# Kernel tuning notes

Hardware: AMD Instinct MI355X
Metric: run time of the kernel (lower is better)

The kernel has to match this reference:

```python
import jax, jax.numpy as jnp
import numpy as np

E = 8        # n_experts
K = 2        # top_k
D = 1024     # n_embed
H = 2048     # moe_n_hidden
B, T = 4, 2048


def setup_inputs() -> dict:
    key = jax.random.key(0)
    ks = jax.random.split(key, 6)
    s = 0.02
    return {
        "x": jax.random.normal(ks[0], (B, T, D), dtype=jnp.float32),
        "Wr": jax.random.normal(ks[1], (D, E), dtype=jnp.float32) * s,   # router weight
        "W1": jax.random.normal(ks[2], (E, D, 2 * H), dtype=jnp.float32) * s,
        "b1": jnp.zeros((E, 2 * H), dtype=jnp.float32),
        "W2": jax.random.normal(ks[3], (E, H, D), dtype=jnp.float32) * s,
        "b2": jnp.zeros((E, D), dtype=jnp.float32),
    }


def reference(x, Wr, W1, b1, W2, b2):
    b, t, d = x.shape
    # router logits (noise=0, temp=1.0)
    z = jnp.einsum('btd,de->bte', x, Wr)                 # [B,T,E]
    vals, idx = jax.lax.top_k(z, K)                      # [B,T,K]
    gates = jax.nn.softmax(vals, axis=-1)                # [B,T,K]
    # combine weights per (token, expert): sum_k gate_k * 1[idx_k == e]
    onehot = jax.nn.one_hot(idx, E, dtype=x.dtype)       # [B,T,K,E]
    comb = jnp.einsum('btk,btke->bte', gates, onehot).reshape(b * t, E)
    xf = x.reshape(b * t, d)                             # [N,D]
    out = jnp.zeros_like(xf)
    for e in range(E):  # fixed small loop over structurally-distinct experts
        ab = xf @ W1[e] + b1[e]                          # [N,2H]
        a, bb = jnp.split(ab, 2, axis=-1)
        h = jax.nn.silu(a) * bb                          # swiGLU
        y = h @ W2[e] + b2[e]                            # [N,D]
        out = out + comb[:, e:e + 1] * y
    return out.reshape(b, t, d)
```

## Files before the change

kernel.cpp:

```cpp
#include <hip/hip_runtime.h>


#define N_TOK 8192
#define DIM   1024
#define HID   2048
#define NEXP  8
#define NK    (N_TOK * 2)
#define MAXT2 72
#define MAXT1 136

typedef __attribute__((ext_vector_type(8))) short short8;
typedef __attribute__((ext_vector_type(4))) float f32x4;

#define BARX() __builtin_amdgcn_s_barrier()
#define FEN()  asm volatile("" ::: "memory")
#define VMW4() asm volatile("s_waitcnt vmcnt(4)" ::: "memory")
#define VMW2() asm volatile("s_waitcnt vmcnt(2)" ::: "memory")
#define VMW0() asm volatile("s_waitcnt vmcnt(0)" ::: "memory")
#define PRIO(p) __builtin_amdgcn_s_setprio(p)

static __device__ __forceinline__ unsigned short f2bf(float f) {
  unsigned int u = __float_as_uint(f);
  u += 0x7fffu + ((u >> 16) & 1u);
  return (unsigned short)(u >> 16);
}

static __device__ __forceinline__ void glds16(const void* g, void* l) {
  __builtin_amdgcn_global_load_lds(
      (const __attribute__((address_space(1))) unsigned int*)g,
      (__attribute__((address_space(3))) unsigned int*)l, 16, 0, 0);
}

__device__ __forceinline__ void transpose_tile(const float* __restrict__ s,
                                               unsigned short* __restrict__ d,
                                               int R, int C, int c0, int r0,
                                               unsigned short (*tT)[68]) {
  int tid = threadIdx.x;
  int c = tid & 63, rq = tid >> 6;
#pragma unroll
  for (int q = 0; q < 4; ++q) {
    int rb = q * 16 + rq * 4;
    ushort4 v;
    v.x = f2bf(s[(size_t)(r0 + rb + 0) * C + c0 + c]);
    v.y = f2bf(s[(size_t)(r0 + rb + 1) * C + c0 + c]);
    v.z = f2bf(s[(size_t)(r0 + rb + 2) * C + c0 + c]);
    v.w = f2bf(s[(size_t)(r0 + rb + 3) * C + c0 + c]);
    *(ushort4*)&tT[c][rb] = v;
  }
  __syncthreads();
#pragma unroll
  for (int it = 0; it < 4; ++it) {
    int idx = it * 256 + tid;
    int cc = idx >> 4;
    int r4 = (idx & 15) * 4;
    *(ushort4*)(d + (size_t)(c0 + cc) * R + r0 + r4) = *(const ushort4*)&tT[cc][r4];
  }
}

__global__ __launch_bounds__(256) void prep_k(
    const float* __restrict__ x, const float* __restrict__ Wr,
    const float* __restrict__ W1, const float* __restrict__ W2,
    unsigned short* __restrict__ w1t, unsigned short* __restrict__ w2t,
    unsigned short* __restrict__ xb, int* __restrict__ te,
    float* __restrict__ tg, float* __restrict__ out) {
  __shared__ unsigned short tT[64][68];
  int bid = blockIdx.x;
  if (bid < 8192) {
    int z = bid >> 10, rem = bid & 1023;
    int c0 = (rem & 63) * 64, r0 = (rem >> 6) * 64;
    transpose_tile(W1 + (size_t)z * DIM * 2 * HID,
                   w1t + (size_t)z * DIM * 2 * HID, DIM, 2 * HID, c0, r0, tT);
  } else if (bid < 12288) {
    int b2 = bid - 8192;
    int z = b2 >> 9, rem = b2 & 511;
    int c0 = (rem & 15) * 64, r0 = (rem >> 4) * 64;
    transpose_tile(W2 + (size_t)z * HID * DIM,
                   w2t + (size_t)z * HID * DIM, HID, DIM, c0, r0, tT);
  } else if (bid < 14336) {
    int n = (bid - 12288) * 4 + (threadIdx.x >> 6);
    int lane = threadIdx.x & 63;
    float z[8];
#pragma unroll
    for (int e = 0; e < 8; ++e) z[e] = 0.f;
    const float* xr = x + (size_t)n * DIM;
    unsigned short* xbr = xb + (size_t)n * DIM;
#pragma unroll 4
    for (int i = 0; i < DIM / 64; ++i) {
      int d = lane + i * 64;
      float xv = xr[d];
      xbr[d] = f2bf(xv);
      float4 w0 = *(const float4*)(Wr + (size_t)d * 8);
      float4 w1 = *(const float4*)(Wr + (size_t)d * 8 + 4);
      z[0] += xv * w0.x; z[1] += xv * w0.y; z[2] += xv * w0.z; z[3] += xv * w0.w;
      z[4] += xv * w1.x; z[5] += xv * w1.y; z[6] += xv * w1.z; z[7] += xv * w1.w;
    }
    for (int off = 32; off; off >>= 1)
#pragma unroll
      for (int e = 0; e < 8; ++e) z[e] += __shfl_down(z[e], off);
    if (lane == 0) {
      int e0 = 0; float v0 = z[0];
#pragma unroll
      for (int e = 1; e < 8; ++e) if (z[e] > v0) { v0 = z[e]; e0 = e; }
      int e1 = -1; float v1 = -3.4e38f;
#pragma unroll
      for (int e = 0; e < 8; ++e) if (e != e0 && z[e] > v1) { v1 = z[e]; e1 = e; }
      float r = expf(v1 - v0);
      float s0 = 1.f / (1.f + r);
      te[n * 2] = e0; te[n * 2 + 1] = e1;
      tg[n * 2] = s0; tg[n * 2 + 1] = r * s0;
    }
  } else {
    int t = bid - 14336;
    float4* o4 = (float4*)out;
    int idx = t * 256 + threadIdx.x;
#pragma unroll
    for (int i = 0; i < 4; ++i) o4[idx + i * 524288] = (float4){0.f, 0.f, 0.f, 0.f};
  }
}

__global__ __launch_bounds__(1024) void sortscan_k(
    const int* __restrict__ te, const float* __restrict__ tg,
    int* __restrict__ offs, int* __restrict__ tl256, int* __restrict__ tl128,
    int* __restrict__ rows, float* __restrict__ rowg) {
  __shared__ int hist[8];
  __shared__ int curs[8];
  int tid = threadIdx.x;
  if (tid < 8) hist[tid] = 0;
  __syncthreads();
  for (int i = tid; i < NK; i += 1024) atomicAdd(&hist[te[i]], 1);
  __syncthreads();
  if (tid == 0) {
    int o = 0, t2 = 0, t1 = 0;
    offs[0] = 0; tl256[0] = 0; tl128[0] = 0;
    for (int e = 0; e < NEXP; ++e) {
      curs[e] = o;
      o += hist[e];
      offs[e + 1] = o;
      t2 += (hist[e] + 255) >> 8;
      tl256[e + 1] = t2;
      t1 += (hist[e] + 127) >> 7;
      tl128[e + 1] = t1;
    }
  }
  __syncthreads();
  for (int i = tid; i < NK; i += 1024) {
    int e = te[i];
    int pos = atomicAdd(&curs[e], 1);
    rows[pos] = i >> 1;
    rowg[pos] = tg[i];
  }
}

template <int GID, int BM>
__global__ __launch_bounds__(512, 2) void moe_gemm8p(
    const unsigned short* __restrict__ Asrc,
    const unsigned short* __restrict__ Wt,
    const float* __restrict__ bias,
    unsigned short* __restrict__ hb,
    float* __restrict__ out,
    const int* __restrict__ rows,
    const float* __restrict__ rowg,
    const int* __restrict__ offs,
    const int* __restrict__ tl) {
  constexpr int KD = (GID == 0) ? DIM : HID;
  constexpr int NT = KD / 64;
  constexpr int MF = BM / 32;
  constexpr int HBIT = BM / 4;
  constexpr int AG = BM / 128;
  constexpr int ASZ = BM * 64;
  __shared__ unsigned short smem[2 * ASZ + 2 * 16384];

  int bt = blockIdx.y;
  if (bt >= tl[NEXP]) return;
  int e = 0;
  while (e < NEXP - 1 && bt >= tl[e + 1]) ++e;
  int rt = bt - tl[e];
  int base = offs[e];
  int cntE = offs[e + 1] - base;
  int row0 = rt * BM;
  int jb = blockIdx.x;

  int tid = threadIdx.x, lane = tid & 63, w = tid >> 6;
  int wr = w >> 2, wc = w & 3;

  int g8 = (((lane & 7) ^ ((lane >> 3) & 7)) * 8);
  const unsigned short* aP[2][AG];
  const unsigned short* bP[2][2];
  int aD[2][AG], bD[2][2];
#pragma unroll
  for (int hf = 0; hf < 2; ++hf) {
#pragma unroll
    for (int s = 0; s < AG; ++s) {
      int q0 = w * (BM / 16) + s * 8;
      int rbA = (q0 < HBIT ? q0 : q0 + HBIT) + hf * HBIT;
      int rA = rbA + (lane >> 3);
      int rr = row0 + rA; rr = rr < cntE ? rr : cntE - 1;
      if (GID == 0) {
        int tok = rows[base + rr];
        aP[hf][s] = Asrc + (size_t)tok * DIM + g8;
      } else {
        aP[hf][s] = Asrc + (size_t)(base + rr) * HID + g8;
      }
      aD[hf][s] = rbA * 64;
    }
#pragma unroll
    for (int s = 0; s < 2; ++s) {
      int q0 = w * 16 + s * 8;
      int rB = hf * 128 + q0 + (lane >> 3);
      if (GID == 0) {
        int j0h = jb * 128;
        int hcol = j0h + (rB >> 5) * 16 + (rB & 15);
        int w1row = hcol + ((rB >> 4) & 1) * HID;
        bP[hf][s] = Wt + ((size_t)e * 2 * HID + w1row) * DIM + g8;
      } else {
        int j0 = jb * 256;
        bP[hf][s] = Wt + ((size_t)e * DIM + (j0 + rB)) * HID + g8;
      }
      bD[hf][s] = (hf * 128 + q0) * 64;
    }
  }

  auto stA = [&](int t, int hf) {
    if (t < NT) {
#pragma unroll
      for (int s = 0; s < AG; ++s)
        glds16(aP[hf][s] + (size_t)t * 64, smem + (t & 1) * ASZ + aD[hf][s]);
    }
  };
  auto stB = [&](int t, int hf) {
    if (t < NT) {
#pragma unroll
      for (int s = 0; s < 2; ++s)
        glds16(bP[hf][s] + (size_t)t * 64, smem + 2 * ASZ + (t & 1) * 16384 + bD[hf][s]);
    }
  };

  int arow = wr * (BM / 2) + (lane & 15);
  int brow = wc * 64 + (lane & 15);
  int kg = lane >> 4, sx = lane & 7;
  unsigned aoffs[2] = {(unsigned)(arow * 64 + ((kg ^ sx) * 8)),
                       (unsigned)(arow * 64 + (((4 + kg) ^ sx) * 8))};
  unsigned boffs[2] = {(unsigned)(brow * 64 + ((kg ^ sx) * 8)),
                       (unsigned)(brow * 64 + (((4 + kg) ^ sx) * 8))};

  f32x4 acc[MF][4];
#pragma unroll
  for (int m = 0; m < MF; ++m)
#pragma unroll
    for (int n = 0; n < 4; ++n) acc[m][n] = (f32x4){0.f, 0.f, 0.f, 0.f};

  short8 a[2][MF / 2], b[2][4];

#define MFMA_Q(MB, NB)                                                        \
  PRIO(1);                                                                    \
  _Pragma("unroll") for (int ks = 0; ks < 2; ++ks)                            \
  _Pragma("unroll") for (int m = 0; m < MF / 2; ++m)                          \
  _Pragma("unroll") for (int n = 0; n < 2; ++n)                               \
    acc[(MB) + m][(NB) + n] = __builtin_amdgcn_mfma_f32_16x16x32_bf16(        \
        a[ks][m], b[ks][(NB) + n], acc[(MB) + m][(NB) + n], 0, 0, 0);         \
  PRIO(0)

#define GUARD_CNT()                                                           \
  if constexpr (BM == 256) { VMW4(); } else { VMW2(); }

  stA(0, 0); stA(0, 1); stB(0, 0); stB(0, 1); stA(1, 0); stA(1, 1);
  GUARD_CNT(); FEN(); BARX(); FEN();

  for (int it = 0; it < NT / 2; ++it) {
    int T = 2 * it;
    bool notlast = (it < NT / 2 - 1);
#pragma unroll
    for (int half = 0; half < 2; ++half) {
      unsigned Ab = half ? (unsigned)ASZ : 0u;
      unsigned Bb = 2u * ASZ + (half ? 16384u : 0u);
      int Tn = T + half;
#pragma unroll
      for (int ks = 0; ks < 2; ++ks) {
#pragma unroll
        for (int m = 0; m < MF / 2; ++m)
          a[ks][m] = *(const short8*)(smem + Ab + aoffs[ks] + m * 1024);
#pragma unroll
        for (int n = 0; n < 2; ++n)
          b[ks][n] = *(const short8*)(smem + Bb + boffs[ks] + n * 1024);
      }
      stB(Tn + 1, 0);
      FEN(); BARX(); FEN();
      MFMA_Q(0, 0);
      FEN(); BARX(); FEN();
#pragma unroll
      for (int ks = 0; ks < 2; ++ks)
#pragma unroll
        for (int n = 2; n < 4; ++n)
          b[ks][n] = *(const short8*)(smem + Bb + boffs[ks] + n * 1024);
      stB(Tn + 1, 1);
      FEN(); BARX(); FEN();
      MFMA_Q(0, 2);
      FEN(); BARX(); FEN();
#pragma unroll
      for (int ks = 0; ks < 2; ++ks)
#pragma unroll
        for (int m = 0; m < MF / 2; ++m)
          a[ks][m] = *(const short8*)(smem + Ab + aoffs[ks] + (MF / 2 + m) * 1024);
      stA(Tn + 2, 0);
      FEN(); BARX(); FEN();
      MFMA_Q(MF / 2, 2);
      FEN(); BARX(); FEN();
      stA(Tn + 2, 1);
      FEN(); BARX(); FEN();
      MFMA_Q(MF / 2, 0);
      if (half == 0) {
        if (notlast) { GUARD_CNT(); } else { VMW0(); }
      } else {
        GUARD_CNT();
      }
      FEN(); BARX(); FEN();
    }
  }
#undef MFMA_Q
#undef GUARD_CNT

  int rowl = lane >> 4, coll = lane & 15;
  if (GID == 0) {
    int j0h = jb * 128;
#pragma unroll
    for (int pair = 0; pair < 2; ++pair) {
      int hcol = j0h + (2 * wc + pair) * 16 + coll;
      float ba = bias[e * 2 * HID + hcol];
      float bb = bias[e * 2 * HID + HID + hcol];
#pragma unroll
      for (int m = 0; m < MF; ++m)
#pragma unroll
        for (int j = 0; j < 4; ++j) {
          int grow = row0 + wr * (BM / 2) + m * 16 + rowl * 4 + j;
          if (grow < cntE) {
            float av = acc[m][2 * pair][j] + ba;
            float bv = acc[m][2 * pair + 1][j] + bb;
            float hv = av / (1.f + __expf(-av)) * bv;
            hb[(size_t)(base + grow) * HID + hcol] = f2bf(hv);
          }
        }
    }
  } else {
    int j0 = jb * 256;
    float bv[4];
#pragma unroll
    for (int n = 0; n < 4; ++n) bv[n] = bias[e * DIM + j0 + wc * 64 + n * 16 + coll];
#pragma unroll
    for (int m = 0; m < MF; ++m)
#pragma unroll
      for (int j = 0; j < 4; ++j) {
        int grow = row0 + wr * (BM / 2) + m * 16 + rowl * 4 + j;
        if (grow < cntE) {
          int tok = rows[base + grow];
          float g = rowg[base + grow];
#pragma unroll
          for (int n = 0; n < 4; ++n) {
            int col = j0 + wc * 64 + n * 16 + coll;
            atomicAdd(&out[(size_t)tok * DIM + col], g * (acc[m][n][j] + bv[n]));
          }
        }
      }
  }
}

extern "C" void kernel_launch(void* const* d_in, const int* in_sizes, int n_in,
                              void* d_out, int out_size, void* d_ws, size_t ws_size,
                              hipStream_t stream) {
  (void)in_sizes; (void)n_in; (void)out_size;
  const float* x  = (const float*)d_in[0];
  const float* Wr = (const float*)d_in[1];
  const float* W1 = (const float*)d_in[2];
  const float* b1 = (const float*)d_in[3];
  const float* W2 = (const float*)d_in[4];
  const float* b2 = (const float*)d_in[5];
  float* out = (float*)d_out;
  char* ws = (char*)d_ws;

  const size_t o_xb   = 0;
  const size_t o_w1t  = o_xb   + (size_t)N_TOK * DIM * 2;
  const size_t o_w2t  = o_w1t  + (size_t)NEXP * 2 * HID * DIM * 2;
  const size_t o_hb   = o_w2t  + (size_t)NEXP * DIM * HID * 2;
  const size_t o_rows = o_hb   + (size_t)NK * HID * 2;
  const size_t o_rowg = o_rows + (size_t)NK * 4;
  const size_t o_te   = o_rowg + (size_t)NK * 4;
  const size_t o_tg   = o_te   + (size_t)NK * 4;
  const size_t o_offs = o_tg   + (size_t)NK * 4;
  const size_t o_t2   = o_offs + 64;
  const size_t o_t1   = o_t2   + 64;
  const size_t need   = o_t1   + 64;
  if (ws_size < need) return;

  unsigned short* xb  = (unsigned short*)(ws + o_xb);
  unsigned short* w1t = (unsigned short*)(ws + o_w1t);
  unsigned short* w2t = (unsigned short*)(ws + o_w2t);
  unsigned short* hb  = (unsigned short*)(ws + o_hb);
  int*   rows = (int*)(ws + o_rows);
  float* rowg = (float*)(ws + o_rowg);
  int*   te   = (int*)(ws + o_te);
  float* tg   = (float*)(ws + o_tg);
  int*   offs = (int*)(ws + o_offs);
  int*   tl256 = (int*)(ws + o_t2);
  int*   tl128 = (int*)(ws + o_t1);

  prep_k<<<16384, 256, 0, stream>>>(x, Wr, W1, W2, w1t, w2t, xb, te, tg, out);
  sortscan_k<<<1, 1024, 0, stream>>>(te, tg, offs, tl256, tl128, rows, rowg);
  moe_gemm8p<0, 256><<<dim3(HID / 128, MAXT2), 512, 0, stream>>>(
      xb, w1t, b1, hb, nullptr, rows, rowg, offs, tl256);
  moe_gemm8p<1, 128><<<dim3(DIM / 256, MAXT1), 512, 0, stream>>>(
      hb, w2t, b2, nullptr, out, rows, rowg, offs, tl128);
}
```

Measured before the change: 413.5 us.

## Move W2 transpose and output zeroing into extra blocks of the first GEMM

The W2 fp32-to-bf16 transpose and the zeroing of the output buffer move out of the prep kernel. They now run as extra auxiliary blocks (blockIdx.y >= MAXT2) appended to the first expert GEMM launch. The aim is to overlap this memory-bound work with the compute-bound GEMM1 and to shorten the prep kernel. The risk is that the auxiliary blocks compete for CUs and bandwidth with the GEMM tiles, and they may be scheduled after the GEMM tiles rather than beside them.

Result: faster. 395.2 us (-4.4%).

```diff
diff --git a/kernel.cpp b/kernel.cpp
--- a/kernel.cpp
+++ b/kernel.cpp
@@ -8,6 +8,7 @@
 #define NK    (N_TOK * 2)
 #define MAXT2 72
 #define MAXT1 136
+#define AUXY  216
 
 typedef __attribute__((ext_vector_type(8))) short short8;
 typedef __attribute__((ext_vector_type(4))) float f32x4;
@@ -57,12 +58,38 @@
   }
 }
 
+__device__ __forceinline__ void transpose_tile512(const float* __restrict__ s,
+                                                  unsigned short* __restrict__ d,
+                                                  int R, int C, int c0, int r0,
+                                                  unsigned short (*tT)[68]) {
+  int tid = threadIdx.x;
+  int c = tid & 63, rq = tid >> 6;
+#pragma unroll
+  for (int q = 0; q < 2; ++q) {
+    int rb = q * 32 + rq * 4;
+    ushort4 v;
+    v.x = f2bf(s[(size_t)(r0 + rb + 0) * C + c0 + c]);
+    v.y = f2bf(s[(size_t)(r0 + rb + 1) * C + c0 + c]);
+    v.z = f2bf(s[(size_t)(r0 + rb + 2) * C + c0 + c]);
+    v.w = f2bf(s[(size_t)(r0 + rb + 3) * C + c0 + c]);
+    *(ushort4*)&tT[c][rb] = v;
+  }
+  __syncthreads();
+#pragma unroll
+  for (int it = 0; it < 2; ++it) {
+    int idx = it * 512 + tid;
+    int cc = idx >> 4;
+    int r4 = (idx & 15) * 4;
+    *(ushort4*)(d + (size_t)(c0 + cc) * R + r0 + r4) = *(const ushort4*)&tT[cc][r4];
+  }
+}
+
 __global__ __launch_bounds__(256) void prep_k(
     const float* __restrict__ x, const float* __restrict__ Wr,
-    const float* __restrict__ W1, const float* __restrict__ W2,
-    unsigned short* __restrict__ w1t, unsigned short* __restrict__ w2t,
+    const float* __restrict__ W1,
+    unsigned short* __restrict__ w1t,
     unsigned short* __restrict__ xb, int* __restrict__ te,
-    float* __restrict__ tg, float* __restrict__ out) {
+    float* __restrict__ tg) {
   __shared__ unsigned short tT[64][68];
   int bid = blockIdx.x;
   if (bid < 8192) {
@@ -70,14 +97,8 @@
     int c0 = (rem & 63) * 64, r0 = (rem >> 6) * 64;
     transpose_tile(W1 + (size_t)z * DIM * 2 * HID,
                    w1t + (size_t)z * DIM * 2 * HID, DIM, 2 * HID, c0, r0, tT);
-  } else if (bid < 12288) {
-    int b2 = bid - 8192;
-    int z = b2 >> 9, rem = b2 & 511;
-    int c0 = (rem & 15) * 64, r0 = (rem >> 4) * 64;
-    transpose_tile(W2 + (size_t)z * HID * DIM,
-                   w2t + (size_t)z * HID * DIM, HID, DIM, c0, r0, tT);
-  } else if (bid < 14336) {
-    int n = (bid - 12288) * 4 + (threadIdx.x >> 6);
+  } else {
+    int n = (bid - 8192) * 4 + (threadIdx.x >> 6);
     int lane = threadIdx.x & 63;
     float z[8];
 #pragma unroll
@@ -109,12 +130,6 @@
       te[n * 2] = e0; te[n * 2 + 1] = e1;
       tg[n * 2] = s0; tg[n * 2 + 1] = r * s0;
     }
-  } else {
-    int t = bid - 14336;
-    float4* o4 = (float4*)out;
-    int idx = t * 256 + threadIdx.x;
-#pragma unroll
-    for (int i = 0; i < 4; ++i) o4[idx + i * 524288] = (float4){0.f, 0.f, 0.f, 0.f};
   }
 }
 
@@ -161,7 +176,10 @@
     const int* __restrict__ rows,
     const float* __restrict__ rowg,
     const int* __restrict__ offs,
-    const int* __restrict__ tl) {
+    const int* __restrict__ tl,
+    const float* __restrict__ W2f,
+    unsigned short* __restrict__ w2td,
+    float* __restrict__ outz) {
   constexpr int KD = (GID == 0) ? DIM : HID;
   constexpr int NT = KD / 64;
   constexpr int MF = BM / 32;
@@ -171,6 +189,28 @@
   __shared__ unsigned short smem[2 * ASZ + 2 * 16384];
 
   int bt = blockIdx.y;
+  if (GID == 0 && bt >= MAXT2) {
+    unsigned short (*tT)[68] = (unsigned short (*)[68])smem;
+    if (bt < 200) {
+      int base_t = ((bt - MAXT2) * 16 + (int)blockIdx.x) * 2;
+#pragma unroll
+      for (int k = 0; k < 2; ++k) {
+        if (k) __syncthreads();
+        int t = base_t + k;
+        int z = t >> 9, rem = t & 511;
+        int c0 = (rem & 15) * 64, r0 = (rem >> 4) * 64;
+        transpose_tile512(W2f + (size_t)z * HID * DIM,
+                          w2td + (size_t)z * HID * DIM, HID, DIM, c0, r0, tT);
+      }
+    } else {
+      int t = (bt - 200) * 16 + (int)blockIdx.x;
+      float4* o4 = (float4*)outz;
+      int idx = t * 512 + threadIdx.x;
+#pragma unroll
+      for (int i = 0; i < 16; ++i) o4[idx + i * 131072] = (float4){0.f, 0.f, 0.f, 0.f};
+    }
+    return;
+  }
   if (bt >= tl[NEXP]) return;
   int e = 0;
   while (e < NEXP - 1 && bt >= tl[e + 1]) ++e;
@@ -402,10 +442,10 @@
   int*   tl256 = (int*)(ws + o_t2);
   int*   tl128 = (int*)(ws + o_t1);
 
-  prep_k<<<16384, 256, 0, stream>>>(x, Wr, W1, W2, w1t, w2t, xb, te, tg, out);
+  prep_k<<<10240, 256, 0, stream>>>(x, Wr, W1, w1t, xb, te, tg);
   sortscan_k<<<1, 1024, 0, stream>>>(te, tg, offs, tl256, tl128, rows, rowg);
-  moe_gemm8p<0, 256><<<dim3(HID / 128, MAXT2), 512, 0, stream>>>(
-      xb, w1t, b1, hb, nullptr, rows, rowg, offs, tl256);
+  moe_gemm8p<0, 256><<<dim3(HID / 128, AUXY), 512, 0, stream>>>(
+      xb, w1t, b1, hb, nullptr, rows, rowg, offs, tl256, W2, w2t, out);
   moe_gemm8p<1, 128><<<dim3(DIM / 256, MAXT1), 512, 0, stream>>>(
-      hb, w2t, b2, nullptr, out, rows, rowg, offs, tl128);
-}
+      hb, w2t, b2, nullptr, out, rows, rowg, offs, tl128, nullptr, nullptr, nullptr);
+}
```
